# Kernel optimization log

Measured on AMD Instinct MI355X. Metric: run time of the kernel, lower is better.

Reference implementation:

```python
import jax, jax.numpy as jnp
import numpy as np

B, C_IN, C_OUT, H, K = 64, 64, 128, 1855, 6


def setup_inputs() -> dict:
    key = jax.random.key(0)
    k1, k2, k3, k4 = jax.random.split(key, 4)
    x = jax.random.normal(k1, (B, C_IN, H), dtype=jnp.float32)
    # neighbor table [H, K]; valid indices first, -1 padding at the end
    neighbors = jax.random.randint(k2, (H, K), 0, H)
    n_boundary = H // 10
    neighbors = neighbors.at[:n_boundary, K - 2:].set(-1)
    weight_center = jax.random.normal(k3, (C_OUT, C_IN), dtype=jnp.float32) / np.sqrt(C_IN).astype(np.float32)
    weight_neighbors = jax.random.normal(k4, (C_OUT, C_IN, K), dtype=jnp.float32) / np.sqrt(C_IN * K).astype(np.float32)
    bias = jnp.zeros((C_OUT,), dtype=jnp.float32)
    return {
        "x": x,
        "neighbors": neighbors,
        "weight_center": weight_center,
        "weight_neighbors": weight_neighbors,
        "bias": bias,
    }


def reference(x, neighbors, weight_center, weight_neighbors, bias):
    # x: [B, C_in, H]; neighbors: [H, K] with -1 = invalid (valid-first ordering)
    mask = neighbors >= 0                               # [H, K]
    idx = jnp.where(mask, neighbors, 0)                 # safe gather indices
    gathered = x[:, :, idx] * mask.astype(x.dtype)[None, None, :, :]  # [B, C_in, H, K]
    center = jnp.einsum('bch,oc->boh', x, weight_center)              # [B, C_out, H]
    neigh = jnp.einsum('bchk,ock->boh', gathered, weight_neighbors)   # [B, C_out, H]
    counts = (1 + mask.sum(axis=-1)).astype(x.dtype)                  # [H]
    return (center + neigh) / counts[None, None, :] + bias[None, :, None]
```

## Files before the change

### kernel.cpp

```cpp
#include <hip/hip_runtime.h>
#include <hip/hip_bf16.h>
#include <stdint.h>

typedef __bf16 bf16x8 __attribute__((ext_vector_type(8)));
typedef float floatx4 __attribute__((ext_vector_type(4)));
typedef unsigned short u16;
typedef unsigned int u32;

#define B_    64
#define CIN   64
#define COUT  128
#define H_    1855
#define KNB   6
#define KTOT  448
#define NSTEPS 14
#define TILE_H 64
#define RS    456
#define NTILES 29

#define XT_OFF   0
#define XT_BYTES ((size_t)H_ * 4096 * 2)
#define WP_OFF   XT_BYTES
#define WP_BYTES ((size_t)COUT * KTOT * 2)
#define FLAG_OFF (WP_OFF + WP_BYTES)

static __device__ inline u16 f32_to_bf16(float f) {
    u32 u = __float_as_uint(f);
    u32 r = (u + 0x7FFFu + ((u >> 16) & 1u)) >> 16;
    return (u16)r;
}
static __device__ inline float bf16_to_f32(u16 b) {
    return __uint_as_float(((u32)b) << 16);
}

__global__ __launch_bounds__(256) void k_detect(const u32* __restrict__ x,
                                                int* __restrict__ flag) {
    __shared__ int votes;
    if (threadIdx.x == 0) votes = 0;
    __syncthreads();
    int cnt = 0;
#pragma unroll
    for (int i = 0; i < 4; ++i) {
        u32 w = x[threadIdx.x * 4 + i];
        u32 e = (w >> 7) & 0xFFu;
        cnt += (e >= 115u && e <= 131u) ? 1 : 0;
    }
    atomicAdd(&votes, cnt);
    __syncthreads();
    if (threadIdx.x == 0) *flag = (votes >= 512) ? 1 : 0;
}

__global__ __launch_bounds__(256) void k_transpose(const void* __restrict__ x,
                                                   u16* __restrict__ xt,
                                                   const int* __restrict__ flag) {
    int isBf = *flag;
    __shared__ u16 tile[64][65];
    int h0  = blockIdx.x * 64;
    int bc0 = blockIdx.y * 64;
    int lane = threadIdx.x & 63;
    int rowq = threadIdx.x >> 6;
#pragma unroll
    for (int i = 0; i < 16; ++i) {
        int row = i * 4 + rowq;
        int h = h0 + lane;
        u16 v = 0;
        if (h < H_) {
            size_t idx = (size_t)(bc0 + row) * H_ + h;
            v = isBf ? ((const u16*)x)[idx] : f32_to_bf16(((const float*)x)[idx]);
        }
        tile[row][lane] = v;
    }
    __syncthreads();
#pragma unroll
    for (int i = 0; i < 16; ++i) {
        int hr = i * 4 + rowq;
        int h = h0 + hr;
        if (h < H_) xt[(size_t)h * 4096 + bc0 + lane] = tile[lane][hr];
    }
}

__global__ __launch_bounds__(256) void k_pack(const void* __restrict__ wc,
                                              const void* __restrict__ wn,
                                              u16* __restrict__ wp,
                                              const int* __restrict__ flag) {
    int isBf = *flag;
    int tg = blockIdx.x * 256 + threadIdx.x;
    if (tg >= COUT * KTOT) return;
    int o = tg / KTOT;
    int rem = tg - o * KTOT;
    int s = rem >> 6, c = rem & 63;
    int srcIdx = (s == 0) ? (o * CIN + c) : ((o * CIN + c) * KNB + (s - 1));
    u16 v;
    if (s == 0) v = isBf ? ((const u16*)wc)[srcIdx] : f32_to_bf16(((const float*)wc)[srcIdx]);
    else        v = isBf ? ((const u16*)wn)[srcIdx] : f32_to_bf16(((const float*)wn)[srcIdx]);
    wp[tg] = v;
}

__global__ __launch_bounds__(256, 2) void k_main(const u16* __restrict__ xt,
                                                 const u16* __restrict__ wp,
                                                 const int* __restrict__ nbr,
                                                 const void* __restrict__ bias,
                                                 const int* __restrict__ flag,
                                                 void* __restrict__ out) {
    __shared__ __align__(16) u16 X[TILE_H * RS];
    __shared__ float cInv[TILE_H];

    int isBf = *flag;
    int tid  = threadIdx.x;
    int b    = blockIdx.x >> 3;
    int slot = blockIdx.x & 7;
    int lane = tid & 63;
    int wave = tid >> 6;
    int col  = lane & 15;
    int quad = lane >> 4;
    int m0w  = wave * 32;

    bf16x8 afrag[2][NSTEPS];
#pragma unroll
    for (int mt = 0; mt < 2; ++mt) {
        int o = m0w + mt * 16 + col;
#pragma unroll
        for (int kk = 0; kk < NSTEPS; ++kk) {
            afrag[mt][kk] = *(const bf16x8*)(wp + o * KTOT + kk * 32 + quad * 8);
        }
    }
    float biasv[2][4];
#pragma unroll
    for (int mt = 0; mt < 2; ++mt)
#pragma unroll
        for (int r = 0; r < 4; ++r) {
            int o = m0w + mt * 16 + quad * 4 + r;
            biasv[mt][r] = isBf ? bf16_to_f32(((const u16*)bias)[o])
                                : ((const float*)bias)[o];
        }

    for (int t = slot; t < NTILES; t += 8) {
        int h0 = t * TILE_H;
        __syncthreads();

        if (tid < TILE_H) {
            int h = h0 + tid;
            int cnt = 1;
            if (h < H_) {
#pragma unroll
                for (int j = 0; j < KNB; ++j) cnt += (nbr[h * KNB + j] >= 0) ? 1 : 0;
            }
            cInv[tid] = 1.0f / (float)cnt;
        }

#pragma unroll
        for (int s = 0; s < 7; ++s) {
#pragma unroll
            for (int r = 0; r < 2; ++r) {
                int idx = r * 256 + tid;
                int hl = idx >> 3;
                int chunk = idx & 7;
                int h = h0 + hl;
                int src = -1;
                if (h < H_) src = (s == 0) ? h : nbr[h * KNB + (s - 1)];
                uint4 v = make_uint4(0u, 0u, 0u, 0u);
                if (src >= 0 && src < H_)
                    v = *(const uint4*)(xt + (size_t)src * 4096 + b * 64 + chunk * 8);
                *(uint4*)(X + hl * RS + s * 64 + chunk * 8) = v;
            }
        }
        __syncthreads();

        floatx4 acc[2][4];
#pragma unroll
        for (int mt = 0; mt < 2; ++mt)
#pragma unroll
            for (int nt = 0; nt < 4; ++nt)
                acc[mt][nt] = (floatx4){0.0f, 0.0f, 0.0f, 0.0f};

#pragma unroll
        for (int kk = 0; kk < NSTEPS; ++kk) {
            bf16x8 bfr[4];
#pragma unroll
            for (int nt = 0; nt < 4; ++nt)
                bfr[nt] = *(const bf16x8*)(X + (nt * 16 + col) * RS + kk * 32 + quad * 8);
#pragma unroll
            for (int mt = 0; mt < 2; ++mt)
#pragma unroll
                for (int nt = 0; nt < 4; ++nt)
                    acc[mt][nt] = __builtin_amdgcn_mfma_f32_16x16x32_bf16(
                        afrag[mt][kk], bfr[nt], acc[mt][nt], 0, 0, 0);
        }

#pragma unroll
        for (int nt = 0; nt < 4; ++nt) {
            int h = h0 + nt * 16 + col;
            if (h < H_) {
                float ic = cInv[nt * 16 + col];
#pragma unroll
                for (int mt = 0; mt < 2; ++mt)
#pragma unroll
                    for (int r = 0; r < 4; ++r) {
                        int o = m0w + mt * 16 + quad * 4 + r;
                        float v = acc[mt][nt][r] * ic + biasv[mt][r];
                        size_t oi = ((size_t)b * COUT + o) * H_ + h;
                        if (isBf) ((u16*)out)[oi] = f32_to_bf16(v);
                        else      ((float*)out)[oi] = v;
                    }
            }
        }
    }
}

extern "C" void kernel_launch(void* const* d_in, const int* in_sizes, int n_in,
                              void* d_out, int out_size, void* d_ws, size_t ws_size,
                              hipStream_t stream) {
    const void* x    = d_in[0];
    const int*  nbr  = (const int*)d_in[1];
    const void* wc   = d_in[2];
    const void* wn   = d_in[3];
    const void* bias = d_in[4];

    u16* xt  = (u16*)((char*)d_ws + XT_OFF);
    u16* wp  = (u16*)((char*)d_ws + WP_OFF);
    int* flg = (int*)((char*)d_ws + FLAG_OFF);

    k_detect<<<dim3(1), dim3(256), 0, stream>>>((const u32*)x, flg);
    k_pack<<<dim3((COUT * KTOT) / 256), dim3(256), 0, stream>>>(wc, wn, wp, flg);
    k_transpose<<<dim3(NTILES, 64), dim3(256), 0, stream>>>(x, xt, flg);
    k_main<<<dim3(512), dim3(256), 0, stream>>>(xt, wp, nbr, bias, flg, (u16*)d_out);
}
```

Measured before the change: 155.6 us.

## Retile main kernel over batch octets and 8-hex tiles, drop dtype detection

Removes the dtype-detection kernel and the runtime bf16/fp32 branches, so the code assumes fp32 inputs. The per-tile neighbor-count reciprocal moves into the pack kernel as a global array. The main kernel now maps each block to 8 batches by 16 hexagons (two 8-hex tiles) instead of one batch by 64-hex tiles, and launches 928 blocks for better parallelism and gather locality. Output stores become strided across batches, with shorter contiguous runs along h.

Result: no change. 155.6 us (-0.0%).

```diff
diff --git a/kernel.cpp b/kernel.cpp
--- a/kernel.cpp
+++ b/kernel.cpp
@@ -1,5 +1,4 @@
 #include <hip/hip_runtime.h>
-#include <hip/hip_bf16.h>
 #include <stdint.h>
 
 typedef __bf16 bf16x8 __attribute__((ext_vector_type(8)));
@@ -7,162 +6,121 @@
 typedef unsigned short u16;
 typedef unsigned int u32;
 
-#define B_    64
 #define CIN   64
 #define COUT  128
 #define H_    1855
 #define KNB   6
 #define KTOT  448
 #define NSTEPS 14
-#define TILE_H 64
 #define RS    456
-#define NTILES 29
-
-#define XT_OFF   0
-#define XT_BYTES ((size_t)H_ * 4096 * 2)
-#define WP_OFF   XT_BYTES
-#define WP_BYTES ((size_t)COUT * KTOT * 2)
-#define FLAG_OFF (WP_OFF + WP_BYTES)
 
 static __device__ inline u16 f32_to_bf16(float f) {
     u32 u = __float_as_uint(f);
     u32 r = (u + 0x7FFFu + ((u >> 16) & 1u)) >> 16;
     return (u16)r;
 }
-static __device__ inline float bf16_to_f32(u16 b) {
-    return __uint_as_float(((u32)b) << 16);
-}
 
-__global__ __launch_bounds__(256) void k_detect(const u32* __restrict__ x,
-                                                int* __restrict__ flag) {
-    __shared__ int votes;
-    if (threadIdx.x == 0) votes = 0;
-    __syncthreads();
-    int cnt = 0;
-#pragma unroll
-    for (int i = 0; i < 4; ++i) {
-        u32 w = x[threadIdx.x * 4 + i];
-        u32 e = (w >> 7) & 0xFFu;
-        cnt += (e >= 115u && e <= 131u) ? 1 : 0;
-    }
-    atomicAdd(&votes, cnt);
-    __syncthreads();
-    if (threadIdx.x == 0) *flag = (votes >= 512) ? 1 : 0;
-}
-
-__global__ __launch_bounds__(256) void k_transpose(const void* __restrict__ x,
-                                                   u16* __restrict__ xt,
-                                                   const int* __restrict__ flag) {
-    int isBf = *flag;
+__global__ __launch_bounds__(256) void k_transpose(const float* __restrict__ x,
+                                                   u16* __restrict__ xt3) {
     __shared__ u16 tile[64][65];
     int h0  = blockIdx.x * 64;
     int bc0 = blockIdx.y * 64;
     int lane = threadIdx.x & 63;
     int rowq = threadIdx.x >> 6;
+    int h = h0 + lane;
+    bool hv = h < H_;
 #pragma unroll
     for (int i = 0; i < 16; ++i) {
         int row = i * 4 + rowq;
-        int h = h0 + lane;
         u16 v = 0;
-        if (h < H_) {
-            size_t idx = (size_t)(bc0 + row) * H_ + h;
-            v = isBf ? ((const u16*)x)[idx] : f32_to_bf16(((const float*)x)[idx]);
-        }
+        if (hv) v = f32_to_bf16(x[(size_t)(bc0 + row) * H_ + h]);
         tile[row][lane] = v;
     }
     __syncthreads();
 #pragma unroll
     for (int i = 0; i < 16; ++i) {
         int hr = i * 4 + rowq;
-        int h = h0 + hr;
-        if (h < H_) xt[(size_t)h * 4096 + bc0 + lane] = tile[lane][hr];
+        int hh = h0 + hr;
+        if (hh < H_) xt3[(size_t)hh * 4096 + bc0 + lane] = tile[lane][hr];
     }
 }
 
-__global__ __launch_bounds__(256) void k_pack(const void* __restrict__ wc,
-                                              const void* __restrict__ wn,
+__global__ __launch_bounds__(256) void k_pack(const float* __restrict__ wc,
+                                              const float* __restrict__ wn,
+                                              const int* __restrict__ nbr,
                                               u16* __restrict__ wp,
-                                              const int* __restrict__ flag) {
-    int isBf = *flag;
+                                              float* __restrict__ cInvG) {
     int tg = blockIdx.x * 256 + threadIdx.x;
+    if (tg < H_) {
+        int cnt = 1;
+#pragma unroll
+        for (int j = 0; j < KNB; ++j) cnt += (nbr[tg * KNB + j] >= 0) ? 1 : 0;
+        cInvG[tg] = 1.0f / (float)cnt;
+    }
     if (tg >= COUT * KTOT) return;
     int o = tg / KTOT;
     int rem = tg - o * KTOT;
     int s = rem >> 6, c = rem & 63;
-    int srcIdx = (s == 0) ? (o * CIN + c) : ((o * CIN + c) * KNB + (s - 1));
-    u16 v;
-    if (s == 0) v = isBf ? ((const u16*)wc)[srcIdx] : f32_to_bf16(((const float*)wc)[srcIdx]);
-    else        v = isBf ? ((const u16*)wn)[srcIdx] : f32_to_bf16(((const float*)wn)[srcIdx]);
-    wp[tg] = v;
+    float v = (s == 0) ? wc[o * CIN + c]
+                       : wn[(o * CIN + c) * KNB + (s - 1)];
+    wp[tg] = f32_to_bf16(v);
 }
 
-__global__ __launch_bounds__(256, 2) void k_main(const u16* __restrict__ xt,
+__global__ __launch_bounds__(256, 2) void k_main(const u16* __restrict__ xt3,
                                                  const u16* __restrict__ wp,
                                                  const int* __restrict__ nbr,
-                                                 const void* __restrict__ bias,
-                                                 const int* __restrict__ flag,
-                                                 void* __restrict__ out) {
-    __shared__ __align__(16) u16 X[TILE_H * RS];
-    __shared__ float cInv[TILE_H];
+                                                 const float* __restrict__ bias,
+                                                 const float* __restrict__ cInvG,
+                                                 float* __restrict__ out) {
+    __shared__ __align__(16) u16 X[29248];
 
-    int isBf = *flag;
     int tid  = threadIdx.x;
-    int b    = blockIdx.x >> 3;
-    int slot = blockIdx.x & 7;
+    int g    = blockIdx.x;
+    int boct = g & 7;
+    int T    = g >> 3;
+    int b0   = boct * 8;
+
     int lane = tid & 63;
     int wave = tid >> 6;
     int col  = lane & 15;
     int quad = lane >> 4;
     int m0w  = wave * 32;
+    int bl   = lane >> 3;
+    int chunk = lane & 7;
 
     bf16x8 afrag[2][NSTEPS];
 #pragma unroll
     for (int mt = 0; mt < 2; ++mt) {
         int o = m0w + mt * 16 + col;
 #pragma unroll
-        for (int kk = 0; kk < NSTEPS; ++kk) {
+        for (int kk = 0; kk < NSTEPS; ++kk)
             afrag[mt][kk] = *(const bf16x8*)(wp + o * KTOT + kk * 32 + quad * 8);
-        }
     }
     float biasv[2][4];
 #pragma unroll
     for (int mt = 0; mt < 2; ++mt)
 #pragma unroll
-        for (int r = 0; r < 4; ++r) {
-            int o = m0w + mt * 16 + quad * 4 + r;
-            biasv[mt][r] = isBf ? bf16_to_f32(((const u16*)bias)[o])
-                                : ((const float*)bias)[o];
-        }
+        for (int r = 0; r < 4; ++r)
+            biasv[mt][r] = bias[m0w + mt * 16 + quad * 4 + r];
 
-    for (int t = slot; t < NTILES; t += 8) {
-        int h0 = t * TILE_H;
+#pragma unroll
+    for (int tt = 0; tt < 2; ++tt) {
+        int t = T * 2 + tt;
+        int h0 = t * 8;
         __syncthreads();
 
-        if (tid < TILE_H) {
-            int h = h0 + tid;
-            int cnt = 1;
-            if (h < H_) {
 #pragma unroll
-                for (int j = 0; j < KNB; ++j) cnt += (nbr[h * KNB + j] >= 0) ? 1 : 0;
-            }
-            cInv[tid] = 1.0f / (float)cnt;
-        }
-
-#pragma unroll
-        for (int s = 0; s < 7; ++s) {
-#pragma unroll
-            for (int r = 0; r < 2; ++r) {
-                int idx = r * 256 + tid;
-                int hl = idx >> 3;
-                int chunk = idx & 7;
-                int h = h0 + hl;
-                int src = -1;
-                if (h < H_) src = (s == 0) ? h : nbr[h * KNB + (s - 1)];
-                uint4 v = make_uint4(0u, 0u, 0u, 0u);
-                if (src >= 0 && src < H_)
-                    v = *(const uint4*)(xt + (size_t)src * 4096 + b * 64 + chunk * 8);
-                *(uint4*)(X + hl * RS + s * 64 + chunk * 8) = v;
-            }
+        for (int i = 0; i < 14; ++i) {
+            int hl = wave * 2 + (i < 7 ? 0 : 1);
+            int s  = (i < 7) ? i : (i - 7);
+            int h  = h0 + hl;
+            int src = -1;
+            if (h < H_) src = (s == 0) ? h : nbr[h * KNB + (s - 1)];
+            uint4 v = make_uint4(0u, 0u, 0u, 0u);
+            if (src >= 0)
+                v = *(const uint4*)(xt3 + (size_t)src * 4096 + (b0 + bl) * 64 + chunk * 8);
+            int n = bl * 8 + hl;
+            *(uint4*)(X + n * RS + bl * 8 + s * 64 + chunk * 8) = v;
         }
         __syncthreads();
 
@@ -173,36 +131,41 @@
             for (int nt = 0; nt < 4; ++nt)
                 acc[mt][nt] = (floatx4){0.0f, 0.0f, 0.0f, 0.0f};
 
+        int rb[4];
+#pragma unroll
+        for (int nt = 0; nt < 4; ++nt) {
+            int n = nt * 16 + col;
+            rb[nt] = n * RS + (n >> 3) * 8 + quad * 8;
+        }
+
 #pragma unroll
         for (int kk = 0; kk < NSTEPS; ++kk) {
-            bf16x8 bfr[4];
 #pragma unroll
-            for (int nt = 0; nt < 4; ++nt)
-                bfr[nt] = *(const bf16x8*)(X + (nt * 16 + col) * RS + kk * 32 + quad * 8);
+            for (int nt = 0; nt < 4; ++nt) {
+                bf16x8 bfr = *(const bf16x8*)(X + rb[nt] + kk * 32);
+                acc[0][nt] = __builtin_amdgcn_mfma_f32_16x16x32_bf16(
+                    afrag[0][kk], bfr, acc[0][nt], 0, 0, 0);
+                acc[1][nt] = __builtin_amdgcn_mfma_f32_16x16x32_bf16(
+                    afrag[1][kk], bfr, acc[1][nt], 0, 0, 0);
+            }
+        }
+
+        int hh = h0 + (col & 7);
+        float ic = cInvG[hh < H_ ? hh : 0];
+        bool hv = hh < H_;
+#pragma unroll
+        for (int nt = 0; nt < 4; ++nt) {
+            int n = nt * 16 + col;
+            size_t rowbase = ((size_t)(b0 + (n >> 3)) * COUT) * H_ + hh;
 #pragma unroll
             for (int mt = 0; mt < 2; ++mt)
 #pragma unroll
-                for (int nt = 0; nt < 4; ++nt)
-                    acc[mt][nt] = __builtin_amdgcn_mfma_f32_16x16x32_bf16(
-                        afrag[mt][kk], bfr[nt], acc[mt][nt], 0, 0, 0);
-        }
-
-#pragma unroll
-        for (int nt = 0; nt < 4; ++nt) {
-            int h = h0 + nt * 16 + col;
-            if (h < H_) {
-                float ic = cInv[nt * 16 + col];
-#pragma unroll
-                for (int mt = 0; mt < 2; ++mt)
-#pragma unroll
-                    for (int r = 0; r < 4; ++r) {
-                        int o = m0w + mt * 16 + quad * 4 + r;
-                        float v = acc[mt][nt][r] * ic + biasv[mt][r];
-                        size_t oi = ((size_t)b * COUT + o) * H_ + h;
-                        if (isBf) ((u16*)out)[oi] = f32_to_bf16(v);
-                        else      ((float*)out)[oi] = v;
-                    }
-            }
+                for (int r = 0; r < 4; ++r) {
+                    int o = m0w + mt * 16 + quad * 4 + r;
+                    if (hv)
+                        out[rowbase + (size_t)o * H_] =
+                            acc[mt][nt][r] * ic + biasv[mt][r];
+                }
         }
     }
 }
@@ -210,18 +173,17 @@
 extern "C" void kernel_launch(void* const* d_in, const int* in_sizes, int n_in,
                               void* d_out, int out_size, void* d_ws, size_t ws_size,
                               hipStream_t stream) {
-    const void* x    = d_in[0];
-    const int*  nbr  = (const int*)d_in[1];
-    const void* wc   = d_in[2];
-    const void* wn   = d_in[3];
-    const void* bias = d_in[4];
+    const float* x    = (const float*)d_in[0];
+    const int*   nbr  = (const int*)d_in[1];
+    const float* wc   = (const float*)d_in[2];
+    const float* wn   = (const float*)d_in[3];
+    const float* bias = (const float*)d_in[4];
 
-    u16* xt  = (u16*)((char*)d_ws + XT_OFF);
-    u16* wp  = (u16*)((char*)d_ws + WP_OFF);
-    int* flg = (int*)((char*)d_ws + FLAG_OFF);
+    u16*   xt3   = (u16*)d_ws;
+    u16*   wp    = (u16*)((char*)d_ws + (size_t)H_ * 4096 * 2);
+    float* cInvG = (float*)((char*)d_ws + (size_t)H_ * 4096 * 2 + (size_t)COUT * KTOT * 2);
 
-    k_detect<<<dim3(1), dim3(256), 0, stream>>>((const u32*)x, flg);
-    k_pack<<<dim3((COUT * KTOT) / 256), dim3(256), 0, stream>>>(wc, wn, wp, flg);
-    k_transpose<<<dim3(NTILES, 64), dim3(256), 0, stream>>>(x, xt, flg);
-    k_main<<<dim3(512), dim3(256), 0, stream>>>(xt, wp, nbr, bias, flg, (u16*)d_out);
+    k_pack<<<dim3((COUT * KTOT) / 256), dim3(256), 0, stream>>>(wc, wn, nbr, wp, cInvG);
+    k_transpose<<<dim3(29, 64), dim3(256), 0, stream>>>(x, xt3);
+    k_main<<<dim3(928), dim3(256), 0, stream>>>(xt3, wp, nbr, bias, cInvG, (float*)d_out);
 }
```
